# Optimization experiments

Measured on AMD Instinct MI355X. Metric: run time of the kernel, lower is better.

The kernel has to match this reference:

```python
import jax, jax.numpy as jnp
import numpy as np

N, E, IN, H, OUT = 100000, 1600000, 128, 128, 64


def setup_inputs() -> dict:
    key = jax.random.key(0)
    ks = jax.random.split(key, 7)
    x = jax.random.normal(ks[0], (N, IN), dtype=jnp.float32)
    edge_index = jax.random.randint(ks[1], (2, E), 0, N, dtype=jnp.int32)
    # Glorot-style scaled params (PyG SAGEConv: lin_l has bias, lin_r does not)
    s1 = 1.0 / np.sqrt(IN)
    s2 = 1.0 / np.sqrt(H)
    W1_l = jax.random.normal(ks[2], (H, IN), dtype=jnp.float32) * s1
    W1_r = jax.random.normal(ks[3], (H, IN), dtype=jnp.float32) * s1
    b1 = jnp.zeros((H,), dtype=jnp.float32)
    W2_l = jax.random.normal(ks[4], (OUT, H), dtype=jnp.float32) * s2
    W2_r = jax.random.normal(ks[5], (OUT, H), dtype=jnp.float32) * s2
    b2 = jnp.zeros((OUT,), dtype=jnp.float32)
    return {"x": x, "W1_l": W1_l, "W1_r": W1_r, "b1": b1,
            "W2_l": W2_l, "W2_r": W2_r, "b2": b2, "edge_index": edge_index}


def _sage_conv(x, edge_index, W_l, W_r, b):
    # mean-aggregate source-node features at target nodes, then linear + root term
    src, dst = edge_index[0], edge_index[1]
    n = x.shape[0]
    msgs = x[src]                                                   # [E, d]
    agg = jax.ops.segment_sum(msgs, dst, num_segments=n)            # [N, d]
    deg = jax.ops.segment_sum(jnp.ones((src.shape[0],), x.dtype), dst, num_segments=n)
    mean = agg / jnp.clip(deg, 1.0)[:, None]                        # zero-deg nodes stay 0
    return mean @ W_l.T + b + x @ W_r.T


def reference(x, W1_l, W1_r, b1, W2_l, W2_r, b2, edge_index):
    h = _sage_conv(x, edge_index, W1_l, W1_r, b1)
    h = jax.nn.relu(h)  # dropout p=0.0 -> identity
    out = _sage_conv(h, edge_index, W2_l, W2_r, b2)
    return out
```

## Files before the change

### kernel.cpp

```cpp
#include <hip/hip_runtime.h>


typedef unsigned int uint32;
typedef short bf16x4 __attribute__((ext_vector_type(4)));
typedef short bf16x8 __attribute__((ext_vector_type(8)));
typedef float f32x16 __attribute__((ext_vector_type(16)));

__device__ __forceinline__ uint32 pack_bf16_rne(float a, float b) {
    uint32 ua = __float_as_uint(a);
    uint32 ub = __float_as_uint(b);
    uint32 ra = (ua + 0x7fffu + ((ua >> 16) & 1u)) >> 16;
    uint32 rb = (ub + 0x7fffu + ((ub >> 16) & 1u)) >> 16;
    return ra | (rb << 16);
}
__device__ __forceinline__ float bf_lo(uint32 v) { return __uint_as_float(v << 16); }
__device__ __forceinline__ float bf_hi(uint32 v) { return __uint_as_float(v & 0xffff0000u); }

__device__ __forceinline__ short rne16(float v, float* back) {
    uint32 u = __float_as_uint(v);
    uint32 r = (u + 0x7fffu + ((u >> 16) & 1u)) >> 16;
    *back = __uint_as_float(r << 16);
    return (short)r;
}

__device__ __forceinline__ bf16x8 mk_bf8(uint2 lo, uint2 hi) {
    union { uint4 u; bf16x8 v; } cv;
    cv.u.x = lo.x; cv.u.y = lo.y; cv.u.z = hi.x; cv.u.w = hi.y;
    return cv.v;
}
__device__ __forceinline__ uint2 shfl32_u2(uint2 v) {
    uint2 r;
    r.x = __shfl_xor(v.x, 32);
    r.y = __shfl_xor(v.y, 32);
    return r;
}

__global__ void k_prep(const float* __restrict__ x, uint32* __restrict__ xb,
                       short* __restrict__ xpH, long n4, int spl,
                       const float* __restrict__ W1l, const float* __restrict__ W1r,
                       const float* __restrict__ W2l, const float* __restrict__ W2r,
                       short* __restrict__ W1pH, short* __restrict__ W1pL,
                       short* __restrict__ W2pH, short* __restrict__ W2pL) {
    long i = (long)blockIdx.x * blockDim.x + threadIdx.x;
    float back;
    if (i < n4) {
        int node = (int)(i >> 5);
        int k4 = ((int)i & 31) * 4;
        float4 v = ((const float4*)x)[i];
        bf16x4 hi4;
        hi4[0] = rne16(v.x, &back);
        hi4[1] = rne16(v.y, &back);
        hi4[2] = rne16(v.z, &back);
        hi4[3] = rne16(v.w, &back);
        uint2 o;
        o.x = (uint32)(unsigned short)hi4[0] | ((uint32)(unsigned short)hi4[1] << 16);
        o.y = (uint32)(unsigned short)hi4[2] | ((uint32)(unsigned short)hi4[3] << 16);
        ((uint2*)xb)[i] = o;
        int c = k4 >> 3;
        *(bf16x4*)&xpH[(size_t)c * spl + (size_t)node * 8 + (k4 & 7)] = hi4;
        return;
    }
    int i2 = (int)(i - n4);
    if (i2 < 32768) {
        int j = i2 >> 8, k = i2 & 255;
        float v = (k < 128) ? W1l[j * 128 + k] : W1r[j * 128 + k - 128];
        float hb;
        short hs = rne16(v, &hb);
        short ls = rne16(v - hb, &back);
        int idx = (k >> 3) * 1024 + j * 8 + (k & 7);
        W1pH[idx] = hs;
        W1pL[idx] = ls;
    } else if (i2 < 32768 + 16384) {
        int i3 = i2 - 32768;
        int j = i3 >> 7, k = i3 & 127;
        float v = (j < 64) ? W2l[j * 128 + k] : W2r[(j - 64) * 128 + k];
        float hb;
        short hs = rne16(v, &hb);
        short ls = rne16(v - hb, &back);
        int idx = (k >> 3) * 1024 + j * 8 + (k & 7);
        W2pH[idx] = hs;
        W2pL[idx] = ls;
    }
}


__global__ void k_bcount(const int* __restrict__ ei, int E, int NB,
                         int* __restrict__ bucket_cnt) {
    __shared__ int hist[1024];
    int t = threadIdx.x;
    for (int i = t; i < NB; i += 256) hist[i] = 0;
    __syncthreads();
    int stride = gridDim.x * 256;
    for (int e = blockIdx.x * 256 + t; e < E; e += stride)
        atomicAdd(&hist[ei[E + e] >> 8], 1);
    __syncthreads();
    for (int i = t; i < NB; i += 256) {
        int c = hist[i];
        if (c) atomicAdd(&bucket_cnt[i], c);
    }
}

__global__ void k_bscan(const int* __restrict__ bucket_cnt, int NB, int E,
                        int* __restrict__ bucket_off, int* __restrict__ bucket_cur) {
    __shared__ int s[1024];
    int t = threadIdx.x;
    int v = (t < NB) ? bucket_cnt[t] : 0;
    s[t] = v;
    __syncthreads();
    for (int o = 1; o < 1024; o <<= 1) {
        int u = (t >= o) ? s[t - o] : 0;
        __syncthreads();
        s[t] += u;
        __syncthreads();
    }
    int ex = s[t] - v;
    if (t < NB) { bucket_off[t] = ex; bucket_cur[t] = ex; }
    if (t == NB - 1) bucket_off[NB] = ex + v;
}

__global__ void k_bscatter(const int* __restrict__ ei, int E, int NB,
                           int* __restrict__ bucket_cur, uint32* __restrict__ eb) {
    __shared__ int hist[1024];
    __shared__ int base[1024];
    int t = threadIdx.x;
    for (int i = t; i < NB; i += 256) hist[i] = 0;
    __syncthreads();
    int stride = gridDim.x * 256;
    for (int e = blockIdx.x * 256 + t; e < E; e += stride)
        atomicAdd(&hist[ei[E + e] >> 8], 1);
    __syncthreads();
    for (int i = t; i < NB; i += 256) {
        int c = hist[i];
        base[i] = c ? atomicAdd(&bucket_cur[i], c) : 0;
        hist[i] = 0;
    }
    __syncthreads();
    for (int e = blockIdx.x * 256 + t; e < E; e += stride) {
        int d = ei[E + e];
        int b = d >> 8;
        int r = atomicAdd(&hist[b], 1);
        eb[base[b] + r] = ((uint32)(d & 255) << 24) | (uint32)ei[e];
    }
}

__global__ void k_bfinal(const uint32* __restrict__ eb,
                         const int* __restrict__ bucket_off,
                         int* __restrict__ row_ptr, int* __restrict__ col,
                         int N, int E) {
    __shared__ int deg[256];
    __shared__ int sc[256];
    __shared__ int cur[256];
    int b = blockIdx.x;
    int t = threadIdx.x;
    int beg = bucket_off[b], end = bucket_off[b + 1];
    deg[t] = 0;
    __syncthreads();
    for (int e = beg + t; e < end; e += 256)
        atomicAdd(&deg[eb[e] >> 24], 1);
    __syncthreads();
    int v = deg[t];
    sc[t] = v;
    __syncthreads();
    for (int o = 1; o < 256; o <<= 1) {
        int u = (t >= o) ? sc[t - o] : 0;
        __syncthreads();
        sc[t] += u;
        __syncthreads();
    }
    int ex = sc[t] - v;
    int node = b * 256 + t;
    if (node < N) row_ptr[node] = beg + ex;
    if (b == gridDim.x - 1 && t == 0) row_ptr[N] = E;
    cur[t] = ex;
    __syncthreads();
    for (int e = beg + t; e < end; e += 256) {
        uint32 u = eb[e];
        int r = atomicAdd(&cur[u >> 24], 1);
        col[beg + r] = (int)(u & 0xFFFFFFu);
    }
}


__global__ void k_agg_mean(const int* __restrict__ rp, const int* __restrict__ col,
                           const uint32* __restrict__ xb,
                           short* __restrict__ mpH, short* __restrict__ mpL,
                           int N, int spl) {
    int node = blockIdx.x * 4 + (threadIdx.x >> 6);
    if (node >= N) return;
    node = __builtin_amdgcn_readfirstlane(node);
    int lane = threadIdx.x & 63;
    int g = lane >> 4;
    int f = lane & 15;
    int beg = rp[node], end = rp[node + 1];
    const uint4* xb4 = (const uint4*)xb;
    float s[8];
#pragma unroll
    for (int j = 0; j < 8; j++) s[j] = 0.f;

#define ACC_RAW(v)                                                      \
    { s[0] += bf_lo(v.x); s[1] += __uint_as_float(v.x);                 \
      s[2] += bf_lo(v.y); s[3] += __uint_as_float(v.y);                 \
      s[4] += bf_lo(v.z); s[5] += __uint_as_float(v.z);                 \
      s[6] += bf_lo(v.w); s[7] += __uint_as_float(v.w); }

    int e = beg;
    for (; e + 16 <= end; e += 16) {
        uint4 cv = *(const uint4*)(col + e + 4 * g);
        uint4 v0 = xb4[(size_t)cv.x * 16 + f];
        uint4 v1 = xb4[(size_t)cv.y * 16 + f];
        uint4 v2 = xb4[(size_t)cv.z * 16 + f];
        uint4 v3 = xb4[(size_t)cv.w * 16 + f];
        ACC_RAW(v0); ACC_RAW(v1); ACC_RAW(v2); ACC_RAW(v3);
    }
    for (; e + 8 <= end; e += 8) {
        uint2 cv = *(const uint2*)(col + e + 2 * g);
        uint4 v0 = xb4[(size_t)cv.x * 16 + f];
        uint4 v1 = xb4[(size_t)cv.y * 16 + f];
        ACC_RAW(v0); ACC_RAW(v1);
    }
    int rem = end - e;
    if (2 * g < rem) {
        uint4 v0 = xb4[(size_t)col[e + 2 * g] * 16 + f];
        ACC_RAW(v0);
    }
    if (2 * g + 1 < rem) {
        uint4 v0 = xb4[(size_t)col[e + 2 * g + 1] * 16 + f];
        ACC_RAW(v0);
    }
#undef ACC_RAW
#pragma unroll
    for (int j = 0; j < 8; j++) {
        s[j] += __shfl_xor(s[j], 16);
        s[j] += __shfl_xor(s[j], 32);
    }
    if (g == 0) {
        float inv = 1.0f / (float)max(end - beg, 1);
        uint32 H[4], L[4];
#pragma unroll
        for (int p = 0; p < 4; p++) {
            float m0 = s[2 * p] * inv, m1 = s[2 * p + 1] * inv;
            float b;
            short h0 = rne16(m0, &b);
            short l0 = rne16(m0 - b, &b);
            short h1 = rne16(m1, &b);
            short l1 = rne16(m1 - b, &b);
            H[p] = (uint32)(unsigned short)h0 | ((uint32)(unsigned short)h1 << 16);
            L[p] = (uint32)(unsigned short)l0 | ((uint32)(unsigned short)l1 << 16);
        }
        size_t idx = (size_t)f * spl + (size_t)node * 8;
        *(uint4*)&mpH[idx] = make_uint4(H[0], H[1], H[2], H[3]);
        *(uint4*)&mpL[idx] = make_uint4(L[0], L[1], L[2], L[3]);
    }
}


__global__ __launch_bounds__(256) void k_mgemm(
        const short* __restrict__ mpH, const short* __restrict__ mpL,
        const short* __restrict__ xpH,
        const short* __restrict__ W1pH, const short* __restrict__ W1pL,
        const short* __restrict__ W2pH, const short* __restrict__ W2pL,
        const float* __restrict__ b1, const float* __restrict__ b2,
        unsigned short* __restrict__ hl, float* __restrict__ hr, int N, int spl) {
    int t = threadIdx.x;
    int w = t >> 6, lane = t & 63;
    int m = lane & 31, hh = lane >> 5;
    int node0 = blockIdx.x * 128;
    int mynode = node0 + 32 * w + m;
    f32x16 acc[4];
#pragma unroll
    for (int i = 0; i < 4; i++)
#pragma unroll
        for (int r = 0; r < 16; r++) acc[i][r] = 0.f;

    for (int kc = 0; kc < 8; kc++) {
        int c = 2 * kc + hh;
        bf16x8 bH = *(const bf16x8*)(mpH + (size_t)c * spl + (size_t)mynode * 8);
        bf16x8 bL = *(const bf16x8*)(mpL + (size_t)c * spl + (size_t)mynode * 8);
#pragma unroll
        for (int jt = 0; jt < 4; jt++) {
            bf16x8 aH = *(const bf16x8*)(W1pH + c * 1024 + (32 * jt + m) * 8);
            bf16x8 aL = *(const bf16x8*)(W1pL + c * 1024 + (32 * jt + m) * 8);
            acc[jt] = __builtin_amdgcn_mfma_f32_32x32x16_bf16(aH, bH, acc[jt], 0, 0, 0);
            acc[jt] = __builtin_amdgcn_mfma_f32_32x32x16_bf16(aL, bH, acc[jt], 0, 0, 0);
            acc[jt] = __builtin_amdgcn_mfma_f32_32x32x16_bf16(aH, bL, acc[jt], 0, 0, 0);
        }
    }
    for (int kc = 0; kc < 8; kc++) {
        int c = 2 * kc + hh;
        bf16x8 bH = *(const bf16x8*)(xpH + (size_t)c * spl + (size_t)mynode * 8);
#pragma unroll
        for (int jt = 0; jt < 4; jt++) {
            bf16x8 aH = *(const bf16x8*)(W1pH + (16 + c) * 1024 + (32 * jt + m) * 8);
            bf16x8 aL = *(const bf16x8*)(W1pL + (16 + c) * 1024 + (32 * jt + m) * 8);
            acc[jt] = __builtin_amdgcn_mfma_f32_32x32x16_bf16(aH, bH, acc[jt], 0, 0, 0);
            acc[jt] = __builtin_amdgcn_mfma_f32_32x32x16_bf16(aL, bH, acc[jt], 0, 0, 0);
        }
    }
    uint2 h4H[16], h4L[16];
#pragma unroll
    for (int jt = 0; jt < 4; jt++) {
#pragma unroll
        for (int rg = 0; rg < 4; rg++) {
            int j0 = 32 * jt + 8 * rg + 4 * hh;
            int c = 4 * jt + rg;
            float4 bv = *(const float4*)(b1 + j0);
            float bb[4] = {bv.x, bv.y, bv.z, bv.w};
            short hs[4], ls[4];
#pragma unroll
            for (int q = 0; q < 4; q++) {
                float v = fmaxf(acc[jt][4 * rg + q] + bb[q], 0.f);
                float back;
                hs[q] = rne16(v, &back);
                ls[q] = rne16(v - back, &back);
            }
            h4H[c].x = (uint32)(unsigned short)hs[0] | ((uint32)(unsigned short)hs[1] << 16);
            h4H[c].y = (uint32)(unsigned short)hs[2] | ((uint32)(unsigned short)hs[3] << 16);
            h4L[c].x = (uint32)(unsigned short)ls[0] | ((uint32)(unsigned short)ls[1] << 16);
            h4L[c].y = (uint32)(unsigned short)ls[2] | ((uint32)(unsigned short)ls[3] << 16);
        }
    }
#pragma unroll
    for (int i = 0; i < 4; i++)
#pragma unroll
        for (int r = 0; r < 16; r++) acc[i][r] = 0.f;
#pragma unroll
    for (int kc = 0; kc < 8; kc++) {
        int c = 2 * kc + hh;
        uint2 mEH = h4H[2 * kc], mOH = h4H[2 * kc + 1];
        uint2 mEL = h4L[2 * kc], mOL = h4L[2 * kc + 1];
        uint2 eEH = shfl32_u2(mEH), eOH = shfl32_u2(mOH);
        uint2 eEL = shfl32_u2(mEL), eOL = shfl32_u2(mOL);
        uint2 loH = hh ? eOH : mEH;
        uint2 hiH = hh ? mOH : eEH;
        uint2 loL = hh ? eOL : mEL;
        uint2 hiL = hh ? mOL : eEL;
        bf16x8 bH = mk_bf8(loH, hiH);
        bf16x8 bL = mk_bf8(loL, hiL);
#pragma unroll
        for (int jt = 0; jt < 4; jt++) {
            bf16x8 aH = *(const bf16x8*)(W2pH + c * 1024 + (32 * jt + m) * 8);
            bf16x8 aL = *(const bf16x8*)(W2pL + c * 1024 + (32 * jt + m) * 8);
            acc[jt] = __builtin_amdgcn_mfma_f32_32x32x16_bf16(aH, bH, acc[jt], 0, 0, 0);
            acc[jt] = __builtin_amdgcn_mfma_f32_32x32x16_bf16(aL, bH, acc[jt], 0, 0, 0);
            acc[jt] = __builtin_amdgcn_mfma_f32_32x32x16_bf16(aH, bL, acc[jt], 0, 0, 0);
        }
    }
    if (mynode >= N) return;
#pragma unroll
    for (int jt = 0; jt < 2; jt++) {
#pragma unroll
        for (int rg = 0; rg < 4; rg++) {
            int j0 = 32 * jt + 8 * rg + 4 * hh;
            uint2 o;
            o.x = pack_bf16_rne(acc[jt][4 * rg + 0], acc[jt][4 * rg + 1]);
            o.y = pack_bf16_rne(acc[jt][4 * rg + 2], acc[jt][4 * rg + 3]);
            *(uint2*)&hl[(size_t)mynode * 64 + j0] = o;
        }
    }
#pragma unroll
    for (int jt = 2; jt < 4; jt++) {
#pragma unroll
        for (int rg = 0; rg < 4; rg++) {
            int j0 = 32 * (jt - 2) + 8 * rg + 4 * hh;
            float4 bv = *(const float4*)(b2 + j0);
            float4 o;
            o.x = acc[jt][4 * rg + 0] + bv.x;
            o.y = acc[jt][4 * rg + 1] + bv.y;
            o.z = acc[jt][4 * rg + 2] + bv.z;
            o.w = acc[jt][4 * rg + 3] + bv.w;
            *(float4*)&hr[(size_t)mynode * 64 + j0] = o;
        }
    }
}


__global__ void k_agg_out(const int* __restrict__ rp, const int* __restrict__ col,
                          const uint32* __restrict__ hl, const float* __restrict__ hr,
                          float* __restrict__ out, int N) {
    int node = blockIdx.x * 4 + (threadIdx.x >> 6);
    if (node >= N) return;
    node = __builtin_amdgcn_readfirstlane(node);
    int lane = threadIdx.x & 63;
    int g = lane >> 3;
    int f = lane & 7;
    int beg = rp[node], end = rp[node + 1];
    const uint4* hl4 = (const uint4*)hl;
    float s[8];
#pragma unroll
    for (int j = 0; j < 8; j++) s[j] = 0.f;

#define ACC_MSK(v)                                          \
    { s[0] += bf_lo(v.x); s[1] += bf_hi(v.x);               \
      s[2] += bf_lo(v.y); s[3] += bf_hi(v.y);               \
      s[4] += bf_lo(v.z); s[5] += bf_hi(v.z);               \
      s[6] += bf_lo(v.w); s[7] += bf_hi(v.w); }

    int e = beg;
    for (; e + 16 <= end; e += 16) {
        uint2 cv = *(const uint2*)(col + e + 2 * g);
        uint4 v0 = hl4[(size_t)cv.x * 8 + f];
        uint4 v1 = hl4[(size_t)cv.y * 8 + f];
        ACC_MSK(v0); ACC_MSK(v1);
    }
    for (; e + 8 <= end; e += 8) {
        uint4 v0 = hl4[(size_t)col[e + g] * 8 + f];
        ACC_MSK(v0);
    }
    int rem = end - e;
    if (g < rem) {
        uint4 v0 = hl4[(size_t)col[e + g] * 8 + f];
        ACC_MSK(v0);
    }
#undef ACC_MSK
#pragma unroll
    for (int j = 0; j < 8; j++) {
        s[j] += __shfl_xor(s[j], 8);
        s[j] += __shfl_xor(s[j], 16);
        s[j] += __shfl_xor(s[j], 32);
    }
    if (g == 0) {
        float inv = 1.0f / (float)max(end - beg, 1);
        const float* hrp = hr + (size_t)node * 64 + f * 8;
        float4 h0 = *(const float4*)(hrp);
        float4 h1 = *(const float4*)(hrp + 4);
        float4 o0, o1;
        o0.x = s[0] * inv + h0.x;
        o0.y = s[1] * inv + h0.y;
        o0.z = s[2] * inv + h0.z;
        o0.w = s[3] * inv + h0.w;
        o1.x = s[4] * inv + h1.x;
        o1.y = s[5] * inv + h1.y;
        o1.z = s[6] * inv + h1.z;
        o1.w = s[7] * inv + h1.w;
        float* op = out + (size_t)node * 64 + f * 8;
        *(float4*)(op) = o0;
        *(float4*)(op + 4) = o1;
    }
}

extern "C" void kernel_launch(void* const* d_in, const int* in_sizes, int n_in,
                              void* d_out, int out_size, void* d_ws, size_t ws_size,
                              hipStream_t stream) {
    const float* x   = (const float*)d_in[0];
    const float* W1l = (const float*)d_in[1];
    const float* W1r = (const float*)d_in[2];
    const float* b1  = (const float*)d_in[3];
    const float* W2l = (const float*)d_in[4];
    const float* W2r = (const float*)d_in[5];
    const float* b2  = (const float*)d_in[6];
    const int*   ei  = (const int*)d_in[7];
    int N = in_sizes[0] / 128;
    int E = in_sizes[7] / 2;
    int NB = (N + 255) >> 8;
    int gb = (N + 127) / 128;
    int Np = gb * 128;
    int spl = Np * 8;
    float* out = (float*)d_out;

    char* w = (char*)d_ws;
    size_t off = 0;
    auto alloc = [&](size_t bytes) -> char* {
        char* p = w + off;
        off += (bytes + 255) & ~(size_t)255;
        return p;
    };
    int*   row_ptr = (int*)alloc((size_t)(N + 1) * 4);
    int*   bcnt    = (int*)alloc((size_t)(NB + 1) * 4);
    int*   boff    = (int*)alloc((size_t)(NB + 1) * 4);
    int*   bcur    = (int*)alloc((size_t)(NB + 1) * 4);
    short* W1pH    = (short*)alloc(32768 * 2);
    short* W1pL    = (short*)alloc(32768 * 2);
    short* W2pH    = (short*)alloc(16384 * 2);
    short* W2pL    = (short*)alloc(16384 * 2);
    int*   col     = (int*)alloc((size_t)E * 4);
    short* xpH     = (short*)alloc((size_t)16 * spl * 2);
    short* mpH     = (short*)alloc((size_t)16 * spl * 2);
    short* mpL     = (short*)alloc((size_t)16 * spl * 2);
    unsigned short* hl = (unsigned short*)alloc((size_t)N * 64 * 2);
    char*  hrxb    = alloc((size_t)Np * 64 * 4);
    uint32* xb = (uint32*)hrxb;
    float*  hr = (float*)hrxb;
    uint32* eb = (uint32*)hl;

    hipMemsetAsync(bcnt, 0, (size_t)NB * 4, stream);
    long n4 = (long)N * 32;
    long prep_items = n4 + 32768 + 16384;
    k_prep<<<(int)((prep_items + 255) / 256), 256, 0, stream>>>(
        x, xb, xpH, n4, spl, W1l, W1r, W2l, W2r, W1pH, W1pL, W2pH, W2pL);
    k_bcount<<<256, 256, 0, stream>>>(ei, E, NB, bcnt);
    k_bscan<<<1, 1024, 0, stream>>>(bcnt, NB, E, boff, bcur);
    k_bscatter<<<128, 256, 0, stream>>>(ei, E, NB, bcur, eb);
    k_bfinal<<<NB, 256, 0, stream>>>(eb, boff, row_ptr, col, N, E);

    int ab = (N + 3) / 4;
    k_agg_mean<<<ab, 256, 0, stream>>>(row_ptr, col, xb, mpH, mpL, N, spl);
    k_mgemm<<<gb, 256, 0, stream>>>(mpH, mpL, xpH, W1pH, W1pL, W2pH, W2pL,
                                    b1, b2, hl, hr, N, spl);
    k_agg_out<<<ab, 256, 0, stream>>>(row_ptr, col, (const uint32*)hl, hr, out, N);
}
```

Before: 383.0 us.

## Split mgemm output columns across waves and exchange hidden tile via LDS

The fused two-layer GEMM kernel now gives each block 32 nodes, and each of its four waves computes one 32-column slice of the hidden layer, where before each wave owned 32 nodes and all 128 columns. The hidden activations (hi/lo bf16 split) are written to shared memory and synchronized so each wave can read the full K for the second GEMM. The cross-lane shuffle path goes away. This cuts the accumulator registers from four MFMA tiles to one, with launch bounds asking for four blocks per CU, to raise occupancy. The cost is four times more blocks, a __syncthreads, LDS traffic, and each wave re-reading the node feature tiles.

```diff
diff --git a/kernel.cpp b/kernel.cpp
--- a/kernel.cpp
+++ b/kernel.cpp
@@ -21,18 +21,6 @@
     uint32 r = (u + 0x7fffu + ((u >> 16) & 1u)) >> 16;
     *back = __uint_as_float(r << 16);
     return (short)r;
-}
-
-__device__ __forceinline__ bf16x8 mk_bf8(uint2 lo, uint2 hi) {
-    union { uint4 u; bf16x8 v; } cv;
-    cv.u.x = lo.x; cv.u.y = lo.y; cv.u.z = hi.x; cv.u.w = hi.y;
-    return cv.v;
-}
-__device__ __forceinline__ uint2 shfl32_u2(uint2 v) {
-    uint2 r;
-    r.x = __shfl_xor(v.x, 32);
-    r.y = __shfl_xor(v.y, 32);
-    return r;
 }
 
 __global__ void k_prep(const float* __restrict__ x, uint32* __restrict__ xb,
@@ -254,120 +242,98 @@
 }
 
 
-__global__ __launch_bounds__(256) void k_mgemm(
+__global__ __launch_bounds__(256, 4) void k_mgemm(
         const short* __restrict__ mpH, const short* __restrict__ mpL,
         const short* __restrict__ xpH,
         const short* __restrict__ W1pH, const short* __restrict__ W1pL,
         const short* __restrict__ W2pH, const short* __restrict__ W2pL,
         const float* __restrict__ b1, const float* __restrict__ b2,
         unsigned short* __restrict__ hl, float* __restrict__ hr, int N, int spl) {
+    __shared__ short hpH[4096];
+    __shared__ short hpL[4096];
     int t = threadIdx.x;
     int w = t >> 6, lane = t & 63;
     int m = lane & 31, hh = lane >> 5;
-    int node0 = blockIdx.x * 128;
-    int mynode = node0 + 32 * w + m;
-    f32x16 acc[4];
-#pragma unroll
-    for (int i = 0; i < 4; i++)
-#pragma unroll
-        for (int r = 0; r < 16; r++) acc[i][r] = 0.f;
-
+    int node0 = blockIdx.x * 32;
+    int mynode = node0 + m;
+    f32x16 acc;
+#pragma unroll
+    for (int r = 0; r < 16; r++) acc[r] = 0.f;
+
+#pragma unroll
     for (int kc = 0; kc < 8; kc++) {
         int c = 2 * kc + hh;
         bf16x8 bH = *(const bf16x8*)(mpH + (size_t)c * spl + (size_t)mynode * 8);
         bf16x8 bL = *(const bf16x8*)(mpL + (size_t)c * spl + (size_t)mynode * 8);
-#pragma unroll
-        for (int jt = 0; jt < 4; jt++) {
-            bf16x8 aH = *(const bf16x8*)(W1pH + c * 1024 + (32 * jt + m) * 8);
-            bf16x8 aL = *(const bf16x8*)(W1pL + c * 1024 + (32 * jt + m) * 8);
-            acc[jt] = __builtin_amdgcn_mfma_f32_32x32x16_bf16(aH, bH, acc[jt], 0, 0, 0);
-            acc[jt] = __builtin_amdgcn_mfma_f32_32x32x16_bf16(aL, bH, acc[jt], 0, 0, 0);
-            acc[jt] = __builtin_amdgcn_mfma_f32_32x32x16_bf16(aH, bL, acc[jt], 0, 0, 0);
+        bf16x8 xH = *(const bf16x8*)(xpH + (size_t)c * spl + (size_t)mynode * 8);
+        bf16x8 aH1 = *(const bf16x8*)(W1pH + c * 1024 + (32 * w + m) * 8);
+        bf16x8 aL1 = *(const bf16x8*)(W1pL + c * 1024 + (32 * w + m) * 8);
+        bf16x8 aH2 = *(const bf16x8*)(W1pH + (16 + c) * 1024 + (32 * w + m) * 8);
+        bf16x8 aL2 = *(const bf16x8*)(W1pL + (16 + c) * 1024 + (32 * w + m) * 8);
+        acc = __builtin_amdgcn_mfma_f32_32x32x16_bf16(aH1, bH, acc, 0, 0, 0);
+        acc = __builtin_amdgcn_mfma_f32_32x32x16_bf16(aL1, bH, acc, 0, 0, 0);
+        acc = __builtin_amdgcn_mfma_f32_32x32x16_bf16(aH1, bL, acc, 0, 0, 0);
+        acc = __builtin_amdgcn_mfma_f32_32x32x16_bf16(aH2, xH, acc, 0, 0, 0);
+        acc = __builtin_amdgcn_mfma_f32_32x32x16_bf16(aL2, xH, acc, 0, 0, 0);
+    }
+
+#pragma unroll
+    for (int rg = 0; rg < 4; rg++) {
+        int j0 = 32 * w + 8 * rg + 4 * hh;
+        float4 bv = *(const float4*)(b1 + j0);
+        float bb[4] = {bv.x, bv.y, bv.z, bv.w};
+        short hs[4], ls[4];
+#pragma unroll
+        for (int q = 0; q < 4; q++) {
+            float v = fmaxf(acc[4 * rg + q] + bb[q], 0.f);
+            float back;
+            hs[q] = rne16(v, &back);
+            ls[q] = rne16(v - back, &back);
         }
-    }
+        uint2 oh, ol;
+        oh.x = (uint32)(unsigned short)hs[0] | ((uint32)(unsigned short)hs[1] << 16);
+        oh.y = (uint32)(unsigned short)hs[2] | ((uint32)(unsigned short)hs[3] << 16);
+        ol.x = (uint32)(unsigned short)ls[0] | ((uint32)(unsigned short)ls[1] << 16);
+        ol.y = (uint32)(unsigned short)ls[2] | ((uint32)(unsigned short)ls[3] << 16);
+        int idx = (4 * w + rg) * 256 + m * 8 + 4 * hh;
+        *(uint2*)&hpH[idx] = oh;
+        *(uint2*)&hpL[idx] = ol;
+    }
+    __syncthreads();
+
+#pragma unroll
+    for (int r = 0; r < 16; r++) acc[r] = 0.f;
+#pragma unroll
     for (int kc = 0; kc < 8; kc++) {
         int c = 2 * kc + hh;
-        bf16x8 bH = *(const bf16x8*)(xpH + (size_t)c * spl + (size_t)mynode * 8);
-#pragma unroll
-        for (int jt = 0; jt < 4; jt++) {
-            bf16x8 aH = *(const bf16x8*)(W1pH + (16 + c) * 1024 + (32 * jt + m) * 8);
-            bf16x8 aL = *(const bf16x8*)(W1pL + (16 + c) * 1024 + (32 * jt + m) * 8);
-            acc[jt] = __builtin_amdgcn_mfma_f32_32x32x16_bf16(aH, bH, acc[jt], 0, 0, 0);
-            acc[jt] = __builtin_amdgcn_mfma_f32_32x32x16_bf16(aL, bH, acc[jt], 0, 0, 0);
-        }
-    }
-    uint2 h4H[16], h4L[16];
-#pragma unroll
-    for (int jt = 0; jt < 4; jt++) {
+        bf16x8 bH = *(const bf16x8*)&hpH[c * 256 + m * 8];
+        bf16x8 bL = *(const bf16x8*)&hpL[c * 256 + m * 8];
+        bf16x8 aH = *(const bf16x8*)(W2pH + c * 1024 + (32 * w + m) * 8);
+        bf16x8 aL = *(const bf16x8*)(W2pL + c * 1024 + (32 * w + m) * 8);
+        acc = __builtin_amdgcn_mfma_f32_32x32x16_bf16(aH, bH, acc, 0, 0, 0);
+        acc = __builtin_amdgcn_mfma_f32_32x32x16_bf16(aL, bH, acc, 0, 0, 0);
+        acc = __builtin_amdgcn_mfma_f32_32x32x16_bf16(aH, bL, acc, 0, 0, 0);
+    }
+    if (mynode >= N) return;
+    if (w < 2) {
 #pragma unroll
         for (int rg = 0; rg < 4; rg++) {
-            int j0 = 32 * jt + 8 * rg + 4 * hh;
-            int c = 4 * jt + rg;
-            float4 bv = *(const float4*)(b1 + j0);
-            float bb[4] = {bv.x, bv.y, bv.z, bv.w};
-            short hs[4], ls[4];
-#pragma unroll
-            for (int q = 0; q < 4; q++) {
-                float v = fmaxf(acc[jt][4 * rg + q] + bb[q], 0.f);
-                float back;
-                hs[q] = rne16(v, &back);
-                ls[q] = rne16(v - back, &back);
-            }
-            h4H[c].x = (uint32)(unsigned short)hs[0] | ((uint32)(unsigned short)hs[1] << 16);
-            h4H[c].y = (uint32)(unsigned short)hs[2] | ((uint32)(unsigned short)hs[3] << 16);
-            h4L[c].x = (uint32)(unsigned short)ls[0] | ((uint32)(unsigned short)ls[1] << 16);
-            h4L[c].y = (uint32)(unsigned short)ls[2] | ((uint32)(unsigned short)ls[3] << 16);
-        }
-    }
-#pragma unroll
-    for (int i = 0; i < 4; i++)
-#pragma unroll
-        for (int r = 0; r < 16; r++) acc[i][r] = 0.f;
-#pragma unroll
-    for (int kc = 0; kc < 8; kc++) {
-        int c = 2 * kc + hh;
-        uint2 mEH = h4H[2 * kc], mOH = h4H[2 * kc + 1];
-        uint2 mEL = h4L[2 * kc], mOL = h4L[2 * kc + 1];
-        uint2 eEH = shfl32_u2(mEH), eOH = shfl32_u2(mOH);
-        uint2 eEL = shfl32_u2(mEL), eOL = shfl32_u2(mOL);
-        uint2 loH = hh ? eOH : mEH;
-        uint2 hiH = hh ? mOH : eEH;
-        uint2 loL = hh ? eOL : mEL;
-        uint2 hiL = hh ? mOL : eEL;
-        bf16x8 bH = mk_bf8(loH, hiH);
-        bf16x8 bL = mk_bf8(loL, hiL);
-#pragma unroll
-        for (int jt = 0; jt < 4; jt++) {
-            bf16x8 aH = *(const bf16x8*)(W2pH + c * 1024 + (32 * jt + m) * 8);
-            bf16x8 aL = *(const bf16x8*)(W2pL + c * 1024 + (32 * jt + m) * 8);
-            acc[jt] = __builtin_amdgcn_mfma_f32_32x32x16_bf16(aH, bH, acc[jt], 0, 0, 0);
-            acc[jt] = __builtin_amdgcn_mfma_f32_32x32x16_bf16(aL, bH, acc[jt], 0, 0, 0);
-            acc[jt] = __builtin_amdgcn_mfma_f32_32x32x16_bf16(aH, bL, acc[jt], 0, 0, 0);
-        }
-    }
-    if (mynode >= N) return;
-#pragma unroll
-    for (int jt = 0; jt < 2; jt++) {
-#pragma unroll
-        for (int rg = 0; rg < 4; rg++) {
-            int j0 = 32 * jt + 8 * rg + 4 * hh;
+            int j0 = 32 * w + 8 * rg + 4 * hh;
             uint2 o;
-            o.x = pack_bf16_rne(acc[jt][4 * rg + 0], acc[jt][4 * rg + 1]);
-            o.y = pack_bf16_rne(acc[jt][4 * rg + 2], acc[jt][4 * rg + 3]);
+            o.x = pack_bf16_rne(acc[4 * rg + 0], acc[4 * rg + 1]);
+            o.y = pack_bf16_rne(acc[4 * rg + 2], acc[4 * rg + 3]);
             *(uint2*)&hl[(size_t)mynode * 64 + j0] = o;
         }
-    }
-#pragma unroll
-    for (int jt = 2; jt < 4; jt++) {
+    } else {
 #pragma unroll
         for (int rg = 0; rg < 4; rg++) {
-            int j0 = 32 * (jt - 2) + 8 * rg + 4 * hh;
+            int j0 = 32 * (w - 2) + 8 * rg + 4 * hh;
             float4 bv = *(const float4*)(b2 + j0);
             float4 o;
-            o.x = acc[jt][4 * rg + 0] + bv.x;
-            o.y = acc[jt][4 * rg + 1] + bv.y;
-            o.z = acc[jt][4 * rg + 2] + bv.z;
-            o.w = acc[jt][4 * rg + 3] + bv.w;
+            o.x = acc[4 * rg + 0] + bv.x;
+            o.y = acc[4 * rg + 1] + bv.y;
+            o.z = acc[4 * rg + 2] + bv.z;
+            o.w = acc[4 * rg + 3] + bv.w;
             *(float4*)&hr[(size_t)mynode * 64 + j0] = o;
         }
     }
@@ -494,7 +460,8 @@
 
     int ab = (N + 3) / 4;
     k_agg_mean<<<ab, 256, 0, stream>>>(row_ptr, col, xb, mpH, mpL, N, spl);
-    k_mgemm<<<gb, 256, 0, stream>>>(mpH, mpL, xpH, W1pH, W1pL, W2pH, W2pL,
+    int mb = (N + 31) / 32;
+    k_mgemm<<<mb, 256, 0, stream>>>(mpH, mpL, xpH, W1pH, W1pL, W2pH, W2pL,
                                     b1, b2, hl, hr, N, spl);
     k_agg_out<<<ab, 256, 0, stream>>>(row_ptr, col, (const uint32*)hl, hr, out, N);
 }
```

Result: faster. 355.9 us (-7.1%).
